# Kernel tuning notes

Measured on AMD Instinct MI355X. Metric: run time of the kernel, lower is better.

The kernel has to match this reference:

```python
import jax, jax.numpy as jnp
import numpy as np

Z_FAR = 1000.0
LAST_DIST = 1e10


def setup_inputs() -> dict:
    key = jax.random.key(0)
    ks = jax.random.split(key, 5)
    B, H, W, P, F = 1, 128, 128, 128, 64
    HW = H * W
    return {
        "sigma": jax.random.normal(ks[0], (B, HW, P), dtype=jnp.float32),
        "feat": jax.random.normal(ks[1], (B, HW, P, F), dtype=jnp.float32),
        "depth": jax.random.uniform(ks[2], (B, HW, P), dtype=jnp.float32),
        "semantic": jax.random.normal(ks[3], (B, HW, P), dtype=jnp.float32),
        "rays_dir": jax.random.normal(ks[4], (B, HW, 3), dtype=jnp.float32),
        "H": H,
        "W": W,
    }


def _volume_weights(z_vals, ray_vector, sigma):
    # dists[i] = z[i+1]-z[i], last dist = LAST_DIST, scaled by |ray|
    dists = jnp.concatenate(
        [z_vals[..., 1:] - z_vals[..., :-1],
         jnp.full_like(z_vals[..., :1], LAST_DIST)], axis=-1)
    dists = dists * jnp.linalg.norm(ray_vector, axis=-1, keepdims=True)
    alpha = 1.0 - jnp.exp(-jax.nn.relu(sigma) * dists)
    trans = jnp.cumprod(
        jnp.concatenate([jnp.ones_like(alpha[..., :1]), 1.0 - alpha + 1e-10],
                        axis=-1), axis=-1)[..., :-1]
    return alpha * trans


def reference(sigma, feat, depth, semantic, rays_dir, H, W):
    B = depth.shape[0]
    # sort_samples: sort every field along the sample axis by depth
    idx = jnp.argsort(depth, axis=-1)                       # [B, HW, P]
    depth_s = jnp.take_along_axis(depth, idx, axis=-1)
    sigma_s = jnp.take_along_axis(sigma, idx, axis=-1)
    semantic_s = jnp.take_along_axis(semantic, idx, axis=-1)
    feat_s = jnp.take_along_axis(feat, idx[..., None], axis=-2)

    weights = _volume_weights(depth_s, rays_dir, sigma_s)   # [B, HW, P]
    feat_map = jnp.sum(weights[..., None] * feat_s, axis=-2)  # [B, HW, F]

    # L1-normalized weights for depth (torch F.normalize p=1, eps=1e-12)
    wd = weights / jnp.maximum(
        jnp.sum(jnp.abs(weights), axis=-1, keepdims=True), 1e-12)
    depth_map = jnp.sum(wd * depth_s, axis=-1, keepdims=True)  # [B, HW, 1]
    depth_map = jnp.clip((depth_map - 0.001) / (Z_FAR - 0.001), 0.0, 1.0)

    depth_map = depth_map.transpose(0, 2, 1).reshape(B, -1, H, W)
    feat_map = feat_map.transpose(0, 2, 1).reshape(B, -1, H, W)
    alpha_map = jnp.sum(weights, axis=-1).reshape(B, 1, H, W)
    return feat_map, depth_map, alpha_map, weights
```

## Files before the change

### kernel.cpp

```cpp
#include <hip/hip_runtime.h>
#include <stdint.h>

#define HW 16384
#define P 128
#define F 64

__global__ __launch_bounds__(256) void nerf_fused_kernel(
    const float* __restrict__ sigma,
    const float* __restrict__ feat,
    const float* __restrict__ depth,
    const float* __restrict__ rays_dir,
    float* __restrict__ out_feat,
    float* __restrict__ out_depth,
    float* __restrict__ out_alpha,
    float* __restrict__ out_weights)
{
    const int r    = blockIdx.x;
    const int tid  = threadIdx.x;
    const int lane = tid & 63;
    const int wv   = tid >> 6;

    __shared__ unsigned long long skey[P];
    __shared__ float  sdep[P];
    __shared__ float  ssig[P];
    __shared__ int    sidx[P];
    __shared__ float  sw[P];
    __shared__ int    srank[256];
    __shared__ int    plist[P];
    __shared__ unsigned long long smask[2];
    __shared__ float  swave[8];
    __shared__ float4 spart[4][16];

    float myd = 0.f, mysig = 0.f;
    if (tid < P) {
        myd   = depth[r * P + tid];
        mysig = sigma[r * P + tid];
    }
    const float rx = rays_dir[r * 3 + 0];
    const float ry = rays_dir[r * 3 + 1];
    const float rz = rays_dir[r * 3 + 2];

    if (tid < P)
        skey[tid] = ((unsigned long long)__float_as_uint(myd) << 32) | (unsigned)tid;
    __syncthreads();

    {
        const int k  = tid & (P - 1);
        const int jb = (tid >> 7) << 6;
        const unsigned long long mk = skey[k];
        int rk = 0;
        #pragma unroll 16
        for (int j = 0; j < 64; ++j)
            rk += (skey[jb + j] < mk) ? 1 : 0;
        srank[tid] = rk;
    }
    __syncthreads();
    if (tid < P) {
        const int rank = srank[tid] + srank[tid + P];
        sdep[rank] = myd;
        ssig[rank] = mysig;
        sidx[rank] = tid;
    }
    __syncthreads();

    float tp = 1.0f, alpha = 0.f, dsort = 0.f;
    if (tid < P) {
        dsort = sdep[tid];
        const float dz = (tid < P - 1) ? (sdep[tid + 1] - dsort) : 1e10f;
        const float rn = sqrtf(rx * rx + ry * ry + rz * rz);
        const float sg = fmaxf(ssig[tid], 0.0f);
        alpha = 1.0f - expf(-sg * dz * rn);
        tp = (1.0f - alpha) + 1e-10f;
    }

    float scan = tp;
    #pragma unroll
    for (int off = 1; off < 64; off <<= 1) {
        const float v = __shfl_up(scan, off);
        if (lane >= off) scan *= v;
    }
    if (lane == 63 && wv < 2) swave[wv] = scan;
    __syncthreads();

    float w = 0.f;
    int   myoff = 0;
    if (tid < P) {
        float excl = __shfl_up(scan, 1);
        if (lane == 0) excl = 1.0f;
        if (wv == 1) excl *= swave[0];
        w = alpha * excl;

        out_weights[r * P + tid] = w;
        sw[sidx[tid]] = w;

        const unsigned long long mask = __ballot(w != 0.0f);
        if (lane == 0) smask[wv] = mask;
        myoff = (int)__popcll(mask & ((1ull << lane) - 1ull));

        float s1 = w, s2 = w * dsort;
        #pragma unroll
        for (int off = 32; off > 0; off >>= 1) {
            s1 += __shfl_xor(s1, off);
            s2 += __shfl_xor(s2, off);
        }
        if (lane == 0) { swave[2 + wv * 2] = s1; swave[3 + wv * 2] = s2; }
    }
    __syncthreads();

    const int M = (int)(__popcll(smask[0]) + __popcll(smask[1]));

    if (tid < P && w != 0.0f) {
        const int rank = myoff + ((wv == 1) ? (int)__popcll(smask[0]) : 0);
        plist[rank] = sidx[tid];
    }

    if (tid == 0) {
        const float sumw  = swave[2] + swave[4];
        const float sumwd = swave[3] + swave[5];
        float dm = sumwd / fmaxf(sumw, 1e-12f);
        dm = (dm - 0.001f) / (1000.0f - 0.001f);
        dm = fminf(fmaxf(dm, 0.0f), 1.0f);
        out_depth[r] = dm;
        out_alpha[r] = sumw;
    }
    __syncthreads();

    const int f4 = tid & 15;
    const int ps = tid >> 4;
    const float4* fp = (const float4*)(feat + (size_t)r * P * F);

    const int jcap = (M > 0) ? (M - 1) : 0;
    int   pj[8];
    float wj[8];
    #pragma unroll
    for (int i = 0; i < 8; ++i) {
        const int idx = i * 16 + ps;
        const int j   = (idx < M) ? idx : jcap;
        const int p   = plist[j] & (P - 1);
        pj[i] = p;
        wj[i] = (idx < M) ? sw[p] : 0.0f;
    }

    float4 fv[8];
    #pragma unroll
    for (int i = 0; i < 8; ++i)
        fv[i] = fp[pj[i] * (F / 4) + f4];

    float4 acc = make_float4(0.f, 0.f, 0.f, 0.f);
    #pragma unroll
    for (int i = 0; i < 8; ++i) {
        acc.x += wj[i] * fv[i].x;
        acc.y += wj[i] * fv[i].y;
        acc.z += wj[i] * fv[i].z;
        acc.w += wj[i] * fv[i].w;
    }
    acc.x += __shfl_xor(acc.x, 16); acc.y += __shfl_xor(acc.y, 16);
    acc.z += __shfl_xor(acc.z, 16); acc.w += __shfl_xor(acc.w, 16);
    acc.x += __shfl_xor(acc.x, 32); acc.y += __shfl_xor(acc.y, 32);
    acc.z += __shfl_xor(acc.z, 32); acc.w += __shfl_xor(acc.w, 32);

    if ((lane >> 4) == 0) spart[wv][f4] = acc;
    __syncthreads();

    if (tid < 16) {
        const float4 a0 = spart[0][tid];
        const float4 a1 = spart[1][tid];
        const float4 a2 = spart[2][tid];
        const float4 a3 = spart[3][tid];
        const int f = tid * 4;
        out_feat[(size_t)(f + 0) * HW + r] = a0.x + a1.x + a2.x + a3.x;
        out_feat[(size_t)(f + 1) * HW + r] = a0.y + a1.y + a2.y + a3.y;
        out_feat[(size_t)(f + 2) * HW + r] = a0.z + a1.z + a2.z + a3.z;
        out_feat[(size_t)(f + 3) * HW + r] = a0.w + a1.w + a2.w + a3.w;
    }
}

extern "C" void kernel_launch(void* const* d_in, const int* in_sizes, int n_in,
                              void* d_out, int out_size, void* d_ws, size_t ws_size,
                              hipStream_t stream) {
    const float* sigma    = (const float*)d_in[0];
    const float* feat     = (const float*)d_in[1];
    const float* depth    = (const float*)d_in[2];
    const float* rays_dir = (const float*)d_in[4];

    float* out = (float*)d_out;
    float* out_feat    = out;
    float* out_depth   = out + (size_t)F * HW;
    float* out_alpha   = out_depth + HW;
    float* out_weights = out_alpha + HW;

    nerf_fused_kernel<<<HW, 256, 0, stream>>>(sigma, feat, depth, rays_dir,
                                              out_feat, out_depth, out_alpha,
                                              out_weights);
}
```

Measured before the change: 60.88 us.

## Process eight rays per block with software-pipelined feature loads over next ray's sort

Each block now handles eight consecutive rays instead of one. The gather of the current ray's feature rows is issued before the next ray's sort, scan and compaction run, so global-load latency overlaps that LDS-heavy prologue. Block syncs are replaced with explicit LDS waitcnt plus s_barrier and sched_barrier fences. This cuts the grid to 2048 blocks, which may lower occupancy and latency hiding across blocks, and it adds register pressure from holding in-flight loads.

```diff
diff --git a/kernel.cpp b/kernel.cpp
--- a/kernel.cpp
+++ b/kernel.cpp
@@ -4,6 +4,119 @@
 #define HW 16384
 #define P 128
 #define F 64
+#define RPB 8
+
+#define BAR_LDS()                                            \
+    do {                                                     \
+        asm volatile("s_waitcnt lgkmcnt(0)" ::: "memory");   \
+        __builtin_amdgcn_sched_barrier(0);                   \
+        __builtin_amdgcn_s_barrier();                        \
+        __builtin_amdgcn_sched_barrier(0);                   \
+    } while (0)
+
+__device__ __forceinline__ void ray_prologue(
+    int r, int tid, int lane, int wv, int ps,
+    float myd, float mysig, float rx, float ry, float rz,
+    unsigned long long* skey, float* sdep, float* ssig, int* sidx,
+    float* sw, int* srank, int* plist, unsigned long long* smask,
+    float* swave,
+    float* __restrict__ out_weights, float* __restrict__ out_depth,
+    float* __restrict__ out_alpha,
+    int pj[8], float wj[8])
+{
+    if (tid < P)
+        skey[tid] = ((unsigned long long)__float_as_uint(myd) << 32) | (unsigned)tid;
+    BAR_LDS();
+
+    {
+        const int k  = tid & (P - 1);
+        const int jb = (tid >> 7) << 6;
+        const unsigned long long mk = skey[k];
+        int rk = 0;
+        #pragma unroll 16
+        for (int j = 0; j < 64; ++j)
+            rk += (skey[jb + j] < mk) ? 1 : 0;
+        srank[tid] = rk;
+    }
+    BAR_LDS();
+    if (tid < P) {
+        const int rank = srank[tid] + srank[tid + P];
+        sdep[rank] = myd;
+        ssig[rank] = mysig;
+        sidx[rank] = tid;
+    }
+    BAR_LDS();
+
+    float tp = 1.0f, alpha = 0.f, dsort = 0.f;
+    if (tid < P) {
+        dsort = sdep[tid];
+        const float dz = (tid < P - 1) ? (sdep[tid + 1] - dsort) : 1e10f;
+        const float rn = sqrtf(rx * rx + ry * ry + rz * rz);
+        const float sg = fmaxf(ssig[tid], 0.0f);
+        alpha = 1.0f - expf(-sg * dz * rn);
+        tp = (1.0f - alpha) + 1e-10f;
+    }
+
+    float scan = tp;
+    #pragma unroll
+    for (int off = 1; off < 64; off <<= 1) {
+        const float v = __shfl_up(scan, off);
+        if (lane >= off) scan *= v;
+    }
+    if (lane == 63 && wv < 2) swave[wv] = scan;
+    BAR_LDS();
+
+    float w = 0.f;
+    int   myoff = 0;
+    if (tid < P) {
+        float excl = __shfl_up(scan, 1);
+        if (lane == 0) excl = 1.0f;
+        if (wv == 1) excl *= swave[0];
+        w = alpha * excl;
+
+        out_weights[(size_t)r * P + tid] = w;
+        sw[sidx[tid]] = w;
+
+        const unsigned long long mask = __ballot(w != 0.0f);
+        if (lane == 0) smask[wv] = mask;
+        myoff = (int)__popcll(mask & ((1ull << lane) - 1ull));
+
+        float s1 = w, s2 = w * dsort;
+        #pragma unroll
+        for (int off = 32; off > 0; off >>= 1) {
+            s1 += __shfl_xor(s1, off);
+            s2 += __shfl_xor(s2, off);
+        }
+        if (lane == 0) { swave[2 + wv * 2] = s1; swave[3 + wv * 2] = s2; }
+    }
+    BAR_LDS();
+
+    const int M = (int)(__popcll(smask[0]) + __popcll(smask[1]));
+    if (tid < P && w != 0.0f) {
+        const int rank = myoff + ((wv == 1) ? (int)__popcll(smask[0]) : 0);
+        plist[rank] = sidx[tid];
+    }
+    if (tid == 0) {
+        const float sumw  = swave[2] + swave[4];
+        const float sumwd = swave[3] + swave[5];
+        float dm = sumwd / fmaxf(sumw, 1e-12f);
+        dm = (dm - 0.001f) / (1000.0f - 0.001f);
+        dm = fminf(fmaxf(dm, 0.0f), 1.0f);
+        out_depth[r] = dm;
+        out_alpha[r] = sumw;
+    }
+    BAR_LDS();
+
+    const int jcap = (M > 0) ? (M - 1) : 0;
+    #pragma unroll
+    for (int i = 0; i < 8; ++i) {
+        const int idx = i * 16 + ps;
+        const int j   = (idx < M) ? idx : jcap;
+        const int p   = plist[j] & (P - 1);
+        pj[i] = p;
+        wj[i] = (idx < M) ? sw[p] : 0.0f;
+    }
+}
 
 __global__ __launch_bounds__(256) void nerf_fused_kernel(
     const float* __restrict__ sigma,
@@ -15,10 +128,12 @@
     float* __restrict__ out_alpha,
     float* __restrict__ out_weights)
 {
-    const int r    = blockIdx.x;
     const int tid  = threadIdx.x;
     const int lane = tid & 63;
     const int wv   = tid >> 6;
+    const int f4   = tid & 15;
+    const int ps   = tid >> 4;
+    const int r0   = blockIdx.x * RPB;
 
     __shared__ unsigned long long skey[P];
     __shared__ float  sdep[P];
@@ -33,145 +148,77 @@
 
     float myd = 0.f, mysig = 0.f;
     if (tid < P) {
-        myd   = depth[r * P + tid];
-        mysig = sigma[r * P + tid];
-    }
-    const float rx = rays_dir[r * 3 + 0];
-    const float ry = rays_dir[r * 3 + 1];
-    const float rz = rays_dir[r * 3 + 2];
-
-    if (tid < P)
-        skey[tid] = ((unsigned long long)__float_as_uint(myd) << 32) | (unsigned)tid;
-    __syncthreads();
-
-    {
-        const int k  = tid & (P - 1);
-        const int jb = (tid >> 7) << 6;
-        const unsigned long long mk = skey[k];
-        int rk = 0;
-        #pragma unroll 16
-        for (int j = 0; j < 64; ++j)
-            rk += (skey[jb + j] < mk) ? 1 : 0;
-        srank[tid] = rk;
-    }
-    __syncthreads();
-    if (tid < P) {
-        const int rank = srank[tid] + srank[tid + P];
-        sdep[rank] = myd;
-        ssig[rank] = mysig;
-        sidx[rank] = tid;
-    }
-    __syncthreads();
-
-    float tp = 1.0f, alpha = 0.f, dsort = 0.f;
-    if (tid < P) {
-        dsort = sdep[tid];
-        const float dz = (tid < P - 1) ? (sdep[tid + 1] - dsort) : 1e10f;
-        const float rn = sqrtf(rx * rx + ry * ry + rz * rz);
-        const float sg = fmaxf(ssig[tid], 0.0f);
-        alpha = 1.0f - expf(-sg * dz * rn);
-        tp = (1.0f - alpha) + 1e-10f;
-    }
-
-    float scan = tp;
-    #pragma unroll
-    for (int off = 1; off < 64; off <<= 1) {
-        const float v = __shfl_up(scan, off);
-        if (lane >= off) scan *= v;
-    }
-    if (lane == 63 && wv < 2) swave[wv] = scan;
-    __syncthreads();
-
-    float w = 0.f;
-    int   myoff = 0;
-    if (tid < P) {
-        float excl = __shfl_up(scan, 1);
-        if (lane == 0) excl = 1.0f;
-        if (wv == 1) excl *= swave[0];
-        w = alpha * excl;
-
-        out_weights[r * P + tid] = w;
-        sw[sidx[tid]] = w;
-
-        const unsigned long long mask = __ballot(w != 0.0f);
-        if (lane == 0) smask[wv] = mask;
-        myoff = (int)__popcll(mask & ((1ull << lane) - 1ull));
-
-        float s1 = w, s2 = w * dsort;
-        #pragma unroll
-        for (int off = 32; off > 0; off >>= 1) {
-            s1 += __shfl_xor(s1, off);
-            s2 += __shfl_xor(s2, off);
-        }
-        if (lane == 0) { swave[2 + wv * 2] = s1; swave[3 + wv * 2] = s2; }
-    }
-    __syncthreads();
-
-    const int M = (int)(__popcll(smask[0]) + __popcll(smask[1]));
-
-    if (tid < P && w != 0.0f) {
-        const int rank = myoff + ((wv == 1) ? (int)__popcll(smask[0]) : 0);
-        plist[rank] = sidx[tid];
-    }
-
-    if (tid == 0) {
-        const float sumw  = swave[2] + swave[4];
-        const float sumwd = swave[3] + swave[5];
-        float dm = sumwd / fmaxf(sumw, 1e-12f);
-        dm = (dm - 0.001f) / (1000.0f - 0.001f);
-        dm = fminf(fmaxf(dm, 0.0f), 1.0f);
-        out_depth[r] = dm;
-        out_alpha[r] = sumw;
-    }
-    __syncthreads();
-
-    const int f4 = tid & 15;
-    const int ps = tid >> 4;
-    const float4* fp = (const float4*)(feat + (size_t)r * P * F);
-
-    const int jcap = (M > 0) ? (M - 1) : 0;
-    int   pj[8];
-    float wj[8];
-    #pragma unroll
-    for (int i = 0; i < 8; ++i) {
-        const int idx = i * 16 + ps;
-        const int j   = (idx < M) ? idx : jcap;
-        const int p   = plist[j] & (P - 1);
-        pj[i] = p;
-        wj[i] = (idx < M) ? sw[p] : 0.0f;
-    }
-
-    float4 fv[8];
-    #pragma unroll
-    for (int i = 0; i < 8; ++i)
-        fv[i] = fp[pj[i] * (F / 4) + f4];
-
-    float4 acc = make_float4(0.f, 0.f, 0.f, 0.f);
-    #pragma unroll
-    for (int i = 0; i < 8; ++i) {
-        acc.x += wj[i] * fv[i].x;
-        acc.y += wj[i] * fv[i].y;
-        acc.z += wj[i] * fv[i].z;
-        acc.w += wj[i] * fv[i].w;
-    }
-    acc.x += __shfl_xor(acc.x, 16); acc.y += __shfl_xor(acc.y, 16);
-    acc.z += __shfl_xor(acc.z, 16); acc.w += __shfl_xor(acc.w, 16);
-    acc.x += __shfl_xor(acc.x, 32); acc.y += __shfl_xor(acc.y, 32);
-    acc.z += __shfl_xor(acc.z, 32); acc.w += __shfl_xor(acc.w, 32);
-
-    if ((lane >> 4) == 0) spart[wv][f4] = acc;
-    __syncthreads();
-
-    if (tid < 16) {
-        const float4 a0 = spart[0][tid];
-        const float4 a1 = spart[1][tid];
-        const float4 a2 = spart[2][tid];
-        const float4 a3 = spart[3][tid];
-        const int f = tid * 4;
-        out_feat[(size_t)(f + 0) * HW + r] = a0.x + a1.x + a2.x + a3.x;
-        out_feat[(size_t)(f + 1) * HW + r] = a0.y + a1.y + a2.y + a3.y;
-        out_feat[(size_t)(f + 2) * HW + r] = a0.z + a1.z + a2.z + a3.z;
-        out_feat[(size_t)(f + 3) * HW + r] = a0.w + a1.w + a2.w + a3.w;
+        myd   = depth[(size_t)r0 * P + tid];
+        mysig = sigma[(size_t)r0 * P + tid];
+    }
+    const float rx0 = rays_dir[r0 * 3 + 0];
+    const float ry0 = rays_dir[r0 * 3 + 1];
+    const float rz0 = rays_dir[r0 * 3 + 2];
+
+    int pj[8]; float wj[8];
+    ray_prologue(r0, tid, lane, wv, ps, myd, mysig, rx0, ry0, rz0,
+                 skey, sdep, ssig, sidx, sw, srank, plist, smask, swave,
+                 out_weights, out_depth, out_alpha, pj, wj);
+
+    for (int i = 0; i < RPB; ++i) {
+        const int r  = r0 + i;
+        const int rp = (i + 1 < RPB) ? (r + 1) : r;
+
+        float mydN = 0.f, mysigN = 0.f;
+        if (tid < P) {
+            mydN   = depth[(size_t)rp * P + tid];
+            mysigN = sigma[(size_t)rp * P + tid];
+        }
+        const float rxN = rays_dir[rp * 3 + 0];
+        const float ryN = rays_dir[rp * 3 + 1];
+        const float rzN = rays_dir[rp * 3 + 2];
+        __builtin_amdgcn_sched_barrier(0);
+
+        const float4* fp = (const float4*)(feat + (size_t)r * P * F);
+        float4 fv[8];
+        #pragma unroll
+        for (int q = 0; q < 8; ++q)
+            fv[q] = fp[pj[q] * (F / 4) + f4];
+        __builtin_amdgcn_sched_barrier(0);
+
+        int pjN[8]; float wjN[8];
+        #pragma unroll
+        for (int q = 0; q < 8; ++q) { pjN[q] = 0; wjN[q] = 0.f; }
+        if (i + 1 < RPB)
+            ray_prologue(r + 1, tid, lane, wv, ps, mydN, mysigN, rxN, ryN, rzN,
+                         skey, sdep, ssig, sidx, sw, srank, plist, smask, swave,
+                         out_weights, out_depth, out_alpha, pjN, wjN);
+
+        float4 acc = make_float4(0.f, 0.f, 0.f, 0.f);
+        #pragma unroll
+        for (int q = 0; q < 8; ++q) {
+            acc.x += wj[q] * fv[q].x;
+            acc.y += wj[q] * fv[q].y;
+            acc.z += wj[q] * fv[q].z;
+            acc.w += wj[q] * fv[q].w;
+        }
+        acc.x += __shfl_xor(acc.x, 16); acc.y += __shfl_xor(acc.y, 16);
+        acc.z += __shfl_xor(acc.z, 16); acc.w += __shfl_xor(acc.w, 16);
+        acc.x += __shfl_xor(acc.x, 32); acc.y += __shfl_xor(acc.y, 32);
+        acc.z += __shfl_xor(acc.z, 32); acc.w += __shfl_xor(acc.w, 32);
+
+        BAR_LDS();
+        if ((lane >> 4) == 0) spart[wv][f4] = acc;
+        BAR_LDS();
+        if (tid < 16) {
+            const float4 a0 = spart[0][tid];
+            const float4 a1 = spart[1][tid];
+            const float4 a2 = spart[2][tid];
+            const float4 a3 = spart[3][tid];
+            const int f = tid * 4;
+            out_feat[(size_t)(f + 0) * HW + r] = a0.x + a1.x + a2.x + a3.x;
+            out_feat[(size_t)(f + 1) * HW + r] = a0.y + a1.y + a2.y + a3.y;
+            out_feat[(size_t)(f + 2) * HW + r] = a0.z + a1.z + a2.z + a3.z;
+            out_feat[(size_t)(f + 3) * HW + r] = a0.w + a1.w + a2.w + a3.w;
+        }
+
+        #pragma unroll
+        for (int q = 0; q < 8; ++q) { pj[q] = pjN[q]; wj[q] = wjN[q]; }
     }
 }
 
@@ -189,7 +236,7 @@
     float* out_alpha   = out_depth + HW;
     float* out_weights = out_alpha + HW;
 
-    nerf_fused_kernel<<<HW, 256, 0, stream>>>(sigma, feat, depth, rays_dir,
-                                              out_feat, out_depth, out_alpha,
-                                              out_weights);
+    nerf_fused_kernel<<<HW / RPB, 256, 0, stream>>>(sigma, feat, depth, rays_dir,
+                                                    out_feat, out_depth, out_alpha,
+                                                    out_weights);
 }
```

Result: slower. 101.3 us (+66.4%).

## Split fused kernel into weights pass and one-wave-per-ray feature gather pass

Applied to the files above, without the earlier changes.

Splits the single fused kernel into two launches. The first sorts samples, computes weights, depth and alpha, and writes compacted nonzero weights with their original sample indices to workspace. The second handles four rays per block, one wave per ray, and loops only over the nonzero entries to gather and accumulate features, so no cross-wave shared-memory reduction is needed. The aim is to shorten the feature gather and drop the block-level sync around it. In exchange it adds a second launch and a global-memory round trip for the compacted weights and indices.

```diff
diff --git a/kernel.cpp b/kernel.cpp
--- a/kernel.cpp
+++ b/kernel.cpp
@@ -5,15 +5,16 @@
 #define P 128
 #define F 64
 
-__global__ __launch_bounds__(256) void nerf_fused_kernel(
+__global__ __launch_bounds__(256) void weights_kernel(
     const float* __restrict__ sigma,
-    const float* __restrict__ feat,
     const float* __restrict__ depth,
     const float* __restrict__ rays_dir,
-    float* __restrict__ out_feat,
+    float* __restrict__ out_weights,
     float* __restrict__ out_depth,
     float* __restrict__ out_alpha,
-    float* __restrict__ out_weights)
+    float* __restrict__ wcomp,
+    unsigned char* __restrict__ pcomp,
+    int* __restrict__ mcnt)
 {
     const int r    = blockIdx.x;
     const int tid  = threadIdx.x;
@@ -26,15 +27,13 @@
     __shared__ int    sidx[P];
     __shared__ float  sw[P];
     __shared__ int    srank[256];
-    __shared__ int    plist[P];
     __shared__ unsigned long long smask[2];
     __shared__ float  swave[8];
-    __shared__ float4 spart[4][16];
 
     float myd = 0.f, mysig = 0.f;
     if (tid < P) {
-        myd   = depth[r * P + tid];
-        mysig = sigma[r * P + tid];
+        myd   = depth[(size_t)r * P + tid];
+        mysig = sigma[(size_t)r * P + tid];
     }
     const float rx = rays_dir[r * 3 + 0];
     const float ry = rays_dir[r * 3 + 1];
@@ -82,20 +81,14 @@
     if (lane == 63 && wv < 2) swave[wv] = scan;
     __syncthreads();
 
-    float w = 0.f;
-    int   myoff = 0;
     if (tid < P) {
         float excl = __shfl_up(scan, 1);
         if (lane == 0) excl = 1.0f;
         if (wv == 1) excl *= swave[0];
-        w = alpha * excl;
-
-        out_weights[r * P + tid] = w;
+        const float w = alpha * excl;
+
+        out_weights[(size_t)r * P + tid] = w;
         sw[sidx[tid]] = w;
-
-        const unsigned long long mask = __ballot(w != 0.0f);
-        if (lane == 0) smask[wv] = mask;
-        myoff = (int)__popcll(mask & ((1ull << lane) - 1ull));
 
         float s1 = w, s2 = w * dsort;
         #pragma unroll
@@ -106,13 +99,6 @@
         if (lane == 0) { swave[2 + wv * 2] = s1; swave[3 + wv * 2] = s2; }
     }
     __syncthreads();
-
-    const int M = (int)(__popcll(smask[0]) + __popcll(smask[1]));
-
-    if (tid < P && w != 0.0f) {
-        const int rank = myoff + ((wv == 1) ? (int)__popcll(smask[0]) : 0);
-        plist[rank] = sidx[tid];
-    }
 
     if (tid == 0) {
         const float sumw  = swave[2] + swave[4];
@@ -123,55 +109,92 @@
         out_depth[r] = dm;
         out_alpha[r] = sumw;
     }
-    __syncthreads();
-
-    const int f4 = tid & 15;
-    const int ps = tid >> 4;
-    const float4* fp = (const float4*)(feat + (size_t)r * P * F);
-
-    const int jcap = (M > 0) ? (M - 1) : 0;
-    int   pj[8];
-    float wj[8];
-    #pragma unroll
-    for (int i = 0; i < 8; ++i) {
-        const int idx = i * 16 + ps;
-        const int j   = (idx < M) ? idx : jcap;
-        const int p   = plist[j] & (P - 1);
-        pj[i] = p;
-        wj[i] = (idx < M) ? sw[p] : 0.0f;
-    }
-
-    float4 fv[8];
-    #pragma unroll
-    for (int i = 0; i < 8; ++i)
-        fv[i] = fp[pj[i] * (F / 4) + f4];
+
+    float worig = 0.f;
+    if (tid < P) {
+        worig = sw[tid];
+        const unsigned long long m2 = __ballot(worig != 0.0f);
+        if (lane == 0) smask[wv] = m2;
+    }
+    __syncthreads();
+
+    if (tid < P) {
+        const unsigned long long m2 = smask[wv];
+        const int off  = (int)__popcll(m2 & ((1ull << lane) - 1ull));
+        const int rank = off + ((wv == 1) ? (int)__popcll(smask[0]) : 0);
+        if (worig != 0.0f) {
+            wcomp[(size_t)r * P + rank] = worig;
+            pcomp[(size_t)r * P + rank] = (unsigned char)tid;
+        }
+        if (tid == 0)
+            mcnt[r] = (int)(__popcll(smask[0]) + __popcll(smask[1]));
+    }
+}
+
+__global__ __launch_bounds__(256) void feat_kernel(
+    const float* __restrict__ feat,
+    const float* __restrict__ wcomp,
+    const unsigned char* __restrict__ pcomp,
+    const int* __restrict__ mcnt,
+    float* __restrict__ out_feat)
+{
+    const int tid   = threadIdx.x;
+    const int wv    = tid >> 6;
+    const int lane  = tid & 63;
+    const int rbase = blockIdx.x * 4;
+
+    __shared__ float         swc[512];
+    __shared__ unsigned char spc[512];
+    __shared__ int           sm[4];
+
+    const size_t base = (size_t)rbase * P;
+    swc[tid]       = wcomp[base + tid];
+    swc[tid + 256] = wcomp[base + tid + 256];
+    if (tid < 128)
+        ((unsigned int*)spc)[tid] = ((const unsigned int*)(pcomp + base))[tid];
+    if (tid < 4) sm[tid] = mcnt[rbase + tid];
+    __syncthreads();
+
+    const int ray  = rbase + wv;
+    const int M    = sm[wv];
+    const int f4   = lane & 15;
+    const int psub = lane >> 4;
+
+    const float4* fp = (const float4*)(feat + (size_t)ray * P * F);
+    const float*         wrow = swc + wv * P;
+    const unsigned char* prow = spc + wv * P;
 
     float4 acc = make_float4(0.f, 0.f, 0.f, 0.f);
-    #pragma unroll
-    for (int i = 0; i < 8; ++i) {
-        acc.x += wj[i] * fv[i].x;
-        acc.y += wj[i] * fv[i].y;
-        acc.z += wj[i] * fv[i].z;
-        acc.w += wj[i] * fv[i].w;
-    }
+    const int cap   = (M > 0) ? (M - 1) : 0;
+    const int niter = (M + 7) >> 3;
+    for (int it = 0; it < niter; ++it) {
+        const int j1 = it * 8 + psub;
+        const int j2 = j1 + 4;
+        const int jj1 = (j1 < M) ? j1 : cap;
+        const int jj2 = (j2 < M) ? j2 : cap;
+        const float w1 = (j1 < M) ? wrow[jj1] : 0.0f;
+        const float w2 = (j2 < M) ? wrow[jj2] : 0.0f;
+        const int p1 = prow[jj1];
+        const int p2 = prow[jj2];
+        const float4 v1 = fp[p1 * (F / 4) + f4];
+        const float4 v2 = fp[p2 * (F / 4) + f4];
+        acc.x += w1 * v1.x; acc.y += w1 * v1.y;
+        acc.z += w1 * v1.z; acc.w += w1 * v1.w;
+        acc.x += w2 * v2.x; acc.y += w2 * v2.y;
+        acc.z += w2 * v2.z; acc.w += w2 * v2.w;
+    }
+
     acc.x += __shfl_xor(acc.x, 16); acc.y += __shfl_xor(acc.y, 16);
     acc.z += __shfl_xor(acc.z, 16); acc.w += __shfl_xor(acc.w, 16);
     acc.x += __shfl_xor(acc.x, 32); acc.y += __shfl_xor(acc.y, 32);
     acc.z += __shfl_xor(acc.z, 32); acc.w += __shfl_xor(acc.w, 32);
 
-    if ((lane >> 4) == 0) spart[wv][f4] = acc;
-    __syncthreads();
-
-    if (tid < 16) {
-        const float4 a0 = spart[0][tid];
-        const float4 a1 = spart[1][tid];
-        const float4 a2 = spart[2][tid];
-        const float4 a3 = spart[3][tid];
-        const int f = tid * 4;
-        out_feat[(size_t)(f + 0) * HW + r] = a0.x + a1.x + a2.x + a3.x;
-        out_feat[(size_t)(f + 1) * HW + r] = a0.y + a1.y + a2.y + a3.y;
-        out_feat[(size_t)(f + 2) * HW + r] = a0.z + a1.z + a2.z + a3.z;
-        out_feat[(size_t)(f + 3) * HW + r] = a0.w + a1.w + a2.w + a3.w;
+    if (psub == 0) {
+        const int f = f4 * 4;
+        out_feat[(size_t)(f + 0) * HW + ray] = acc.x;
+        out_feat[(size_t)(f + 1) * HW + ray] = acc.y;
+        out_feat[(size_t)(f + 2) * HW + ray] = acc.z;
+        out_feat[(size_t)(f + 3) * HW + ray] = acc.w;
     }
 }
 
@@ -189,7 +212,12 @@
     float* out_alpha   = out_depth + HW;
     float* out_weights = out_alpha + HW;
 
-    nerf_fused_kernel<<<HW, 256, 0, stream>>>(sigma, feat, depth, rays_dir,
-                                              out_feat, out_depth, out_alpha,
-                                              out_weights);
+    float*         wcomp = (float*)d_ws;
+    unsigned char* pcomp = (unsigned char*)d_ws + (size_t)HW * P * 4;
+    int*           mcnt  = (int*)((unsigned char*)d_ws + (size_t)HW * P * 5);
+
+    weights_kernel<<<HW, 256, 0, stream>>>(sigma, depth, rays_dir,
+                                           out_weights, out_depth, out_alpha,
+                                           wcomp, pcomp, mcnt);
+    feat_kernel<<<HW / 4, 256, 0, stream>>>(feat, wcomp, pcomp, mcnt, out_feat);
 }
```

Result: slower. 91.17 us (+49.8%).
